# Kernel tuning notes

Hardware: AMD Instinct MI355X
Metric: run time of the kernel (lower is better)

Reference implementation:

```python
import jax, jax.numpy as jnp
import numpy as np

WINDOW_LENGTH = 128
PAD = WINDOW_LENGTH // 2  # ReflectionPad1d(window_length/2)


def _hanning(w_len, dtype):
    n = jnp.arange(w_len, dtype=jnp.float32)
    w = 0.5 - 0.5 * jnp.cos(2.0 * jnp.pi * n / (w_len - 1))
    return w.astype(dtype)


def setup_inputs() -> dict:
    key = jax.random.key(0)
    seq = jax.random.normal(key, (16, 512, 64), dtype=jnp.float32)
    return {"seq": seq}


def reference(seq):
    B, L, C = seq.shape
    w = _hanning(WINDOW_LENGTH, seq.dtype)  # [W]
    # reflection pad along time, then strided framing via a gather (replaces the cat loop)
    padded = jnp.pad(seq, ((0, 0), (PAD, PAD), (0, 0)), mode="reflect")  # [B, L+2*PAD, C]
    idx = jnp.arange(L)[:, None] + jnp.arange(WINDOW_LENGTH)[None, :]  # [L, W]
    frames = padded[:, idx, :] * w[None, None, :, None]  # [B, L, W, C]
    cube = jnp.fft.rfft(frames, axis=2)  # [B, L, F=W//2+1, C] complex64
    # complex standardization over dims (1, 2): zero-mean, unit second moment per (batch, channel)
    mu = jnp.mean(cube, axis=(1, 2), keepdims=True)
    centered = cube - mu
    std = jnp.sqrt(jnp.mean(jnp.abs(centered) ** 2, axis=(1, 2), keepdims=True))
    normed = centered / std
    return jnp.abs(normed)  # amplitude of the standardized freq cube, [B, L, F, C]
```

## Files before the change

### kernel.cpp

```cpp
#include <hip/hip_runtime.h>
#include <math.h>


#define B_ 16
#define L_ 512
#define C_ 64
#define W_ 128
#define F_ 65
#define LP 640
#define NLF (L_ * F_)

constexpr double kPI = 3.14159265358979323846;

constexpr double csin_(double x) {
  while (x > kPI) x -= 2.0 * kPI;
  while (x < -kPI) x += 2.0 * kPI;
  double t = x, s = x, x2 = x * x;
  for (int i = 1; i <= 24; ++i) {
    t *= -x2 / ((2.0 * i) * (2.0 * i + 1.0));
    s += t;
  }
  return s;
}
constexpr double ccos_(double x) { return csin_(kPI / 2.0 - x); }

constexpr int bitrev6(int n) {
  int r = 0;
  for (int i = 0; i < 6; ++i) r |= ((n >> i) & 1) << (5 - i);
  return r;
}

struct Tables {
  float win[128];
  float walt[128];
  float w2[128];
  float wg[128];
  float twr[32], twi[32];
  float cur[32], cui[32];
  constexpr Tables() : win(), walt(), w2(), wg(), twr(), twi(), cur(), cui() {
    for (int n = 0; n < 128; ++n) {
      const double wd = 0.5 - 0.5 * ccos_(2.0 * kPI * n / 127.0);
      win[n] = (float)wd;
      walt[n] = (n & 1) ? (float)(-wd) : (float)wd;
      w2[n] = (float)(wd * wd);
      if (n == 0) {
        wg[n] = 0.0f;
      } else {
        const double G = csin_(kPI * n / 2.0) * csin_(65.0 * kPI * n / 128.0) /
                         csin_(kPI * n / 128.0);
        wg[n] = (float)(wd * G);
      }
    }
    for (int j = 0; j < 32; ++j) {
      twr[j] = (float)ccos_(2.0 * kPI * j / 64.0);
      twi[j] = (float)(-csin_(2.0 * kPI * j / 64.0));
    }
    for (int k = 0; k < 32; ++k) {
      cur[k] = (float)ccos_(2.0 * kPI * k / 128.0);
      cui[k] = (float)(-csin_(2.0 * kPI * k / 128.0));
    }
  }
};
constexpr Tables TBL{};

__device__ __forceinline__ int refl(int t) {
  const int a = max(t, -t);
  return min(a, 1022 - a);
}

__device__ __forceinline__ float fast_sqrt(float x) {
  float r;
  asm("v_sqrt_f32 %0, %1" : "=v"(r) : "v"(x));
  return r;
}

__device__ __forceinline__ float2 cmul(float wr, float wi, float2 v) {
  return make_float2(__builtin_fmaf(wi, -v.y, wr * v.x),
                     __builtin_fmaf(wi, v.x, wr * v.y));
}

__global__ void __launch_bounds__(256)
fe_pad_kernel(const float* __restrict__ seq, float* __restrict__ pad,
              float* __restrict__ acc) {
  const int idx = blockIdx.x * 256 + threadIdx.x;
  if (idx < 3072) acc[idx] = 0.0f;
  const int c = idx & 63;
  const int row = idx >> 6;
  const int b = row / LP;
  const int t = row - b * LP;
  const int s = refl(t - 64);
  pad[idx] = seq[(b * L_ + s) * C_ + c];
}

__global__ void __launch_bounds__(256)
fe_reduce_kernel(const float* __restrict__ pad, float* __restrict__ acc) {
  const int p = blockIdx.x * 4 + (threadIdx.x >> 6);
  const int b = __builtin_amdgcn_readfirstlane(p >> 9);
  const int l = __builtin_amdgcn_readfirstlane(p & (L_ - 1));
  const int c = threadIdx.x & 63;

  const float* base = pad + ((size_t)(b * LP + l)) * C_ + c;

  float2 a0 = make_float2(0.f, 0.f), a1 = a0, a2 = a0, a3 = a0;
#pragma unroll
  for (int n = 0; n < 64; ++n) {
    const float2 v = make_float2(base[(2 * n) * C_], base[(2 * n + 1) * C_]);
    a0.x = __builtin_fmaf(TBL.win[2 * n], v.x, a0.x);
    a0.y = __builtin_fmaf(TBL.win[2 * n + 1], v.y, a0.y);
    a1.x = __builtin_fmaf(TBL.walt[2 * n], v.x, a1.x);
    a1.y = __builtin_fmaf(TBL.walt[2 * n + 1], v.y, a1.y);
    const float2 wv = make_float2(TBL.w2[2 * n] * v.x, TBL.w2[2 * n + 1] * v.y);
    a2.x = __builtin_fmaf(wv.x, v.x, a2.x);
    a2.y = __builtin_fmaf(wv.y, v.y, a2.y);
    a3.x = __builtin_fmaf(TBL.wg[2 * n], v.x, a3.x);
    a3.y = __builtin_fmaf(TBL.wg[2 * n + 1], v.y, a3.y);
  }
  const float x0 = a0.x + a0.y;
  const float x64 = a1.x + a1.y;
  const float p2 = a2.x + a2.y;
  const float d2 = a3.x + a3.y;

  const float sre = 0.5f * (x0 + x64);
  const float sim = -d2;
  const float ssq = 64.0f * p2 + 0.5f * (x0 * x0 + x64 * x64);

  __shared__ float red[3][256];
  const int tid = threadIdx.x;
  red[0][tid] = sre;
  red[1][tid] = sim;
  red[2][tid] = ssq;
  __syncthreads();
  if (tid < 64) {
    const float a0s = red[0][tid] + red[0][tid + 64] + red[0][tid + 128] + red[0][tid + 192];
    const float a1s = red[1][tid] + red[1][tid + 64] + red[1][tid + 128] + red[1][tid + 192];
    const float a2s = red[2][tid] + red[2][tid + 64] + red[2][tid + 128] + red[2][tid + 192];
    const int g = b * C_ + tid;
    unsafeAtomicAdd(&acc[g], a0s);
    unsafeAtomicAdd(&acc[1024 + g], a1s);
    unsafeAtomicAdd(&acc[2048 + g], a2s);
  }
}

__global__ void __launch_bounds__(256, 3)
fe_write_kernel(const float* __restrict__ pad, const float* __restrict__ acc,
                float* __restrict__ out) {
  const int tid = threadIdx.x;
  const int p = blockIdx.x * 4 + (tid >> 6);
  const int b = __builtin_amdgcn_readfirstlane(p >> 9);
  const int l = __builtin_amdgcn_readfirstlane(p & (L_ - 1));
  const int c = tid & 63;

  const int g = b * C_ + c;
  const float invN = 1.0f / (float)NLF;
  const float sr = acc[g] * invN;
  const float si = acc[1024 + g] * invN;
  const float qq = acc[2048 + g] * invN;
  const float var = qq - sr * sr - si * si;
  const float2 mu = make_float2(2.0f * sr, 2.0f * si);
  const float is = 0.5f * rsqrtf(var);

  const float* base = pad + ((size_t)(b * LP + l)) * C_ + c;

  float2 z[64];
#pragma unroll
  for (int n = 0; n < 64; ++n) {
    const int m = bitrev6(n);
    z[n] = make_float2(TBL.win[2 * m] * base[(2 * m) * C_],
                       TBL.win[2 * m + 1] * base[(2 * m + 1) * C_]);
  }

#pragma unroll
  for (int s = 0; s < 6; ++s) {
    const int half = 1 << s;
    const int len = half << 1;
#pragma unroll
    for (int j = 0; j < half; ++j) {
      const float wr = TBL.twr[j << (5 - s)];
      const float wi = TBL.twi[j << (5 - s)];
#pragma unroll
      for (int base2 = 0; base2 < 64; base2 += len) {
        const int a = base2 + j;
        const int b2 = a + half;
        const float2 t = cmul(wr, wi, z[b2]);
        const float2 za = z[a];
        z[b2] = make_float2(za.x - t.x, za.y - t.y);
        z[a] = make_float2(za.x + t.x, za.y + t.y);
      }
    }
  }

  float* obase = out + (((size_t)(b * L_ + l)) * F_) * C_ + c;
  auto emit = [&](int f, float2 X) {
    const float2 d = make_float2(X.x - mu.x, X.y - mu.y);
    const float amp =
        fast_sqrt(__builtin_fmaf(d.x, d.x, d.y * d.y)) * is;
    __builtin_nontemporal_store(amp, &obase[(size_t)f * C_]);
  };

  emit(0, make_float2(2.0f * (z[0].x + z[0].y), 0.0f));
  emit(64, make_float2(2.0f * (z[0].x - z[0].y), 0.0f));
  emit(32, make_float2(2.0f * z[32].x, -2.0f * z[32].y));
#pragma unroll
  for (int k = 1; k < 32; ++k) {
    const float2 zk = z[k], zm = z[64 - k];
    const float2 e = make_float2(zk.x + zm.x, zk.y - zm.y);
    const float2 o = make_float2(zk.y + zm.y, zm.x - zk.x);
    const float2 wO = cmul(TBL.cur[k], TBL.cui[k], o);
    emit(k, make_float2(e.x + wO.x, e.y + wO.y));
    emit(64 - k, make_float2(e.x - wO.x, wO.y - e.y));
  }
}

extern "C" void kernel_launch(void* const* d_in, const int* in_sizes, int n_in,
                              void* d_out, int out_size, void* d_ws, size_t ws_size,
                              hipStream_t stream) {
  const float* seq = (const float*)d_in[0];
  float* out = (float*)d_out;
  float* ws = (float*)d_ws;
  float* acc = ws;
  float* pad = ws + 4096;

  fe_pad_kernel<<<(B_ * LP * C_) / 256, 256, 0, stream>>>(seq, pad, acc);
  const int nblocks = (B_ * L_) / 4;
  fe_reduce_kernel<<<nblocks, 256, 0, stream>>>(pad, acc);
  fe_write_kernel<<<nblocks, 256, 0, stream>>>(pad, acc, out);
}
```

Baseline: 57.17 us.

## Replace per-thread radix-2 FFT with fp16 MFMA windowed DFT matmul

The write kernel no longer runs a per-thread 64-point complex FFT with a real-FFT post-pass. Instead it computes the windowed real DFT as a matrix product: a constexpr fp16 matrix of window-scaled cos/sin rows (144x128) is multiplied by fp16 frame data through 16x16x32 MFMA instructions, and the standardisation and amplitude are applied to the accumulator outputs. This is meant to remove the heavy FP32 butterfly ALU work and register pressure of the FFT. It loses precision by casting both the inputs and the DFT coefficients to fp16, does redundant DFT work compared with an FFT, and reads the A matrix from constant memory on every tile.

```diff
diff --git a/kernel.cpp b/kernel.cpp
--- a/kernel.cpp
+++ b/kernel.cpp
@@ -10,6 +10,9 @@
 #define LP 640
 #define NLF (L_ * F_)
 
+typedef _Float16 half8 __attribute__((ext_vector_type(8)));
+typedef float f32x4 __attribute__((ext_vector_type(4)));
+
 constexpr double kPI = 3.14159265358979323846;
 
 constexpr double csin_(double x) {
@@ -24,20 +27,12 @@
 }
 constexpr double ccos_(double x) { return csin_(kPI / 2.0 - x); }
 
-constexpr int bitrev6(int n) {
-  int r = 0;
-  for (int i = 0; i < 6; ++i) r |= ((n >> i) & 1) << (5 - i);
-  return r;
-}
-
 struct Tables {
   float win[128];
   float walt[128];
   float w2[128];
   float wg[128];
-  float twr[32], twi[32];
-  float cur[32], cui[32];
-  constexpr Tables() : win(), walt(), w2(), wg(), twr(), twi(), cur(), cui() {
+  constexpr Tables() : win(), walt(), w2(), wg() {
     for (int n = 0; n < 128; ++n) {
       const double wd = 0.5 - 0.5 * ccos_(2.0 * kPI * n / 127.0);
       win[n] = (float)wd;
@@ -51,17 +46,29 @@
         wg[n] = (float)(wd * G);
       }
     }
-    for (int j = 0; j < 32; ++j) {
-      twr[j] = (float)ccos_(2.0 * kPI * j / 64.0);
-      twi[j] = (float)(-csin_(2.0 * kPI * j / 64.0));
-    }
-    for (int k = 0; k < 32; ++k) {
-      cur[k] = (float)ccos_(2.0 * kPI * k / 128.0);
-      cui[k] = (float)(-csin_(2.0 * kPI * k / 128.0));
-    }
   }
 };
 constexpr Tables TBL{};
+
+struct alignas(16) AMat {
+  _Float16 a[144][128];
+  constexpr AMat() : a() {
+    double cs[128] = {}, sn[128] = {}, w[128] = {};
+    for (int m = 0; m < 128; ++m) {
+      cs[m] = ccos_(2.0 * kPI * m / 128.0);
+      sn[m] = csin_(2.0 * kPI * m / 128.0);
+    }
+    for (int n = 0; n < 128; ++n)
+      w[n] = 0.5 - 0.5 * ccos_(2.0 * kPI * n / 127.0);
+    for (int f = 0; f <= 64; ++f)
+      for (int n = 0; n < 128; ++n) {
+        const int m = (f * n) & 127;
+        a[2 * f][n] = (_Float16)(cs[m] * w[n]);
+        a[2 * f + 1][n] = (_Float16)(-sn[m] * w[n]);
+      }
+  }
+};
+constexpr AMat AMT{};
 
 __device__ __forceinline__ int refl(int t) {
   const int a = max(t, -t);
@@ -72,11 +79,6 @@
   float r;
   asm("v_sqrt_f32 %0, %1" : "=v"(r) : "v"(x));
   return r;
-}
-
-__device__ __forceinline__ float2 cmul(float wr, float wi, float2 v) {
-  return make_float2(__builtin_fmaf(wi, -v.y, wr * v.x),
-                     __builtin_fmaf(wi, v.x, wr * v.y));
 }
 
 __global__ void __launch_bounds__(256)
@@ -141,73 +143,81 @@
   }
 }
 
-__global__ void __launch_bounds__(256, 3)
+__global__ void __launch_bounds__(256)
 fe_write_kernel(const float* __restrict__ pad, const float* __restrict__ acc,
                 float* __restrict__ out) {
   const int tid = threadIdx.x;
   const int p = blockIdx.x * 4 + (tid >> 6);
   const int b = __builtin_amdgcn_readfirstlane(p >> 9);
   const int l = __builtin_amdgcn_readfirstlane(p & (L_ - 1));
-  const int c = tid & 63;
-
-  const int g = b * C_ + c;
+  const int lane = tid & 63;
+  const int m16 = lane & 15;
+  const int g8 = lane >> 4;
+
+  const float* pb = pad + (size_t)(b * LP + l) * C_;
+
+  half8 bf[4][4];
+#pragma unroll
+  for (int kk = 0; kk < 4; ++kk) {
+#pragma unroll
+    for (int nt = 0; nt < 4; ++nt) {
+      const float* q = pb + (kk * 32 + g8 * 8) * C_ + nt * 16 + m16;
+      half8 v;
+#pragma unroll
+      for (int j = 0; j < 8; ++j) v[j] = (_Float16)q[j * C_];
+      bf[kk][nt] = v;
+    }
+  }
+
+  float mr[4], mi[4], isv[4];
   const float invN = 1.0f / (float)NLF;
-  const float sr = acc[g] * invN;
-  const float si = acc[1024 + g] * invN;
-  const float qq = acc[2048 + g] * invN;
-  const float var = qq - sr * sr - si * si;
-  const float2 mu = make_float2(2.0f * sr, 2.0f * si);
-  const float is = 0.5f * rsqrtf(var);
-
-  const float* base = pad + ((size_t)(b * LP + l)) * C_ + c;
-
-  float2 z[64];
-#pragma unroll
-  for (int n = 0; n < 64; ++n) {
-    const int m = bitrev6(n);
-    z[n] = make_float2(TBL.win[2 * m] * base[(2 * m) * C_],
-                       TBL.win[2 * m + 1] * base[(2 * m + 1) * C_]);
-  }
-
-#pragma unroll
-  for (int s = 0; s < 6; ++s) {
-    const int half = 1 << s;
-    const int len = half << 1;
-#pragma unroll
-    for (int j = 0; j < half; ++j) {
-      const float wr = TBL.twr[j << (5 - s)];
-      const float wi = TBL.twi[j << (5 - s)];
-#pragma unroll
-      for (int base2 = 0; base2 < 64; base2 += len) {
-        const int a = base2 + j;
-        const int b2 = a + half;
-        const float2 t = cmul(wr, wi, z[b2]);
-        const float2 za = z[a];
-        z[b2] = make_float2(za.x - t.x, za.y - t.y);
-        z[a] = make_float2(za.x + t.x, za.y + t.y);
-      }
-    }
-  }
-
-  float* obase = out + (((size_t)(b * L_ + l)) * F_) * C_ + c;
-  auto emit = [&](int f, float2 X) {
-    const float2 d = make_float2(X.x - mu.x, X.y - mu.y);
-    const float amp =
-        fast_sqrt(__builtin_fmaf(d.x, d.x, d.y * d.y)) * is;
-    __builtin_nontemporal_store(amp, &obase[(size_t)f * C_]);
-  };
-
-  emit(0, make_float2(2.0f * (z[0].x + z[0].y), 0.0f));
-  emit(64, make_float2(2.0f * (z[0].x - z[0].y), 0.0f));
-  emit(32, make_float2(2.0f * z[32].x, -2.0f * z[32].y));
-#pragma unroll
-  for (int k = 1; k < 32; ++k) {
-    const float2 zk = z[k], zm = z[64 - k];
-    const float2 e = make_float2(zk.x + zm.x, zk.y - zm.y);
-    const float2 o = make_float2(zk.y + zm.y, zm.x - zk.x);
-    const float2 wO = cmul(TBL.cur[k], TBL.cui[k], o);
-    emit(k, make_float2(e.x + wO.x, e.y + wO.y));
-    emit(64 - k, make_float2(e.x - wO.x, wO.y - e.y));
+#pragma unroll
+  for (int nt = 0; nt < 4; ++nt) {
+    const int g = b * C_ + nt * 16 + m16;
+    const float sr = acc[g] * invN;
+    const float si = acc[1024 + g] * invN;
+    const float qq = acc[2048 + g] * invN;
+    mr[nt] = sr;
+    mi[nt] = si;
+    isv[nt] = rsqrtf(qq - sr * sr - si * si);
+  }
+
+  float* ob = out + ((size_t)(b * L_ + l) * F_) * C_;
+
+#pragma unroll
+  for (int mt = 0; mt < 9; ++mt) {
+    f32x4 av[4] = {{0.f, 0.f, 0.f, 0.f},
+                   {0.f, 0.f, 0.f, 0.f},
+                   {0.f, 0.f, 0.f, 0.f},
+                   {0.f, 0.f, 0.f, 0.f}};
+#pragma unroll
+    for (int kk = 0; kk < 4; ++kk) {
+      const half8 af =
+          *(const half8*)(&AMT.a[mt * 16 + m16][kk * 32 + g8 * 8]);
+#pragma unroll
+      for (int nt = 0; nt < 4; ++nt)
+        av[nt] = __builtin_amdgcn_mfma_f32_16x16x32_f16(af, bf[kk][nt],
+                                                        av[nt], 0, 0, 0);
+    }
+    const int f0 = mt * 8 + g8 * 2;
+#pragma unroll
+    for (int nt = 0; nt < 4; ++nt) {
+      const int co = nt * 16 + m16;
+      {
+        const float dr = av[nt][0] - mr[nt];
+        const float di = av[nt][1] - mi[nt];
+        const float amp = fast_sqrt(__builtin_fmaf(dr, dr, di * di)) * isv[nt];
+        if (f0 < F_)
+          __builtin_nontemporal_store(amp, ob + (size_t)f0 * C_ + co);
+      }
+      {
+        const float dr = av[nt][2] - mr[nt];
+        const float di = av[nt][3] - mi[nt];
+        const float amp = fast_sqrt(__builtin_fmaf(dr, dr, di * di)) * isv[nt];
+        if (f0 + 1 < F_)
+          __builtin_nontemporal_store(amp, ob + (size_t)(f0 + 1) * C_ + co);
+      }
+    }
   }
 }
 
```

Result: slower. 70.39 us (+23.1%).
